# Kernel tuning notes

Measured on AMD Instinct MI355X. Metric: run time of the kernel, lower is better.

Reference implementation:

```python
import jax, jax.numpy as jnp
import numpy as np

# B groups, N packed tokens/group, D model dim, H heads, L layers, FF mlp hidden,
# M samples packed per group, C classes, PD patch_dim, NF/NT freq/time pos tables
B, N, D, H, L, FF, M, C, PD, NF, NT = 4, 1024, 768, 12, 12, 3072, 8, 527, 256, 8, 64


def _ln(x, g, b, eps=1e-6):
    m = jnp.mean(x, -1, keepdims=True)
    v = jnp.mean((x - m) ** 2, -1, keepdims=True)
    return (x - m) * jax.lax.rsqrt(v + eps) * g + b


def _attn(xq, xkv, Wq, bq, Wkv, bkv, Wo, bo, allowed):
    # allowed: [b, i, j] bool; faithful to source: NO 1/sqrt(d_head) scaling.
    b, i, _ = xq.shape
    j = xkv.shape[1]
    q = (xq @ Wq + bq).reshape(b, i, H, -1).transpose(0, 2, 1, 3)
    k, v = jnp.split(xkv @ Wkv + bkv, 2, axis=-1)
    k = k.reshape(b, j, H, -1).transpose(0, 2, 1, 3)
    v = v.reshape(b, j, H, -1).transpose(0, 2, 1, 3)
    dots = jnp.einsum('bhid,bhjd->bhij', q, k)
    neg = -jnp.finfo(dots.dtype).max
    dots = jnp.where(allowed[:, None, :, :], dots, neg)
    a = jax.nn.softmax(dots, axis=-1)
    out = jnp.einsum('bhij,bhjd->bhid', a, v).transpose(0, 2, 1, 3).reshape(b, i, -1)
    return out @ Wo + bo


def setup_inputs() -> dict:
    ks = iter(jax.random.split(jax.random.key(0), 48))
    rn = lambda shape, s=0.02: jax.random.normal(next(ks), shape, jnp.float32) * s
    return {
        'patches': jax.random.normal(next(ks), (B, N, PD), jnp.float32),
        'sample_ids': jnp.sort(jax.random.randint(next(ks), (B, N), 0, M), axis=-1).astype(jnp.int32),
        'key_pad': jnp.ones((B, N), bool),
        'freq_idx': jax.random.randint(next(ks), (B, N), 0, NF).astype(jnp.int32),
        'time_idx': jax.random.randint(next(ks), (B, N), 0, NT).astype(jnp.int32),
        'patch_W': rn((PD, D)), 'patch_b': jnp.zeros((D,)),
        'pos_f': rn((NF, D), 1.0), 'pos_t': rn((NT, D), 1.0),
        'ln1_g': jnp.ones((L, D)), 'ln1_b': jnp.zeros((L, D)),
        'Wq': rn((L, D, D)), 'bq': jnp.zeros((L, D)),
        'Wkv': rn((L, D, 2 * D)), 'bkv': jnp.zeros((L, 2 * D)),
        'Wo': rn((L, D, D)), 'bo': jnp.zeros((L, D)),
        'ln2_g': jnp.ones((L, D)), 'ln2_b': jnp.zeros((L, D)),
        'W1': rn((L, D, FF)), 'b1': jnp.zeros((L, FF)),
        'W2': rn((L, FF, D)), 'b2': jnp.zeros((L, D)),
        'norm_g': jnp.ones((D,)), 'norm_b': jnp.zeros((D,)),
        'pool_q': rn((D,), 1.0),
        'pool_Wq': rn((D, D)), 'pool_bq': jnp.zeros((D,)),
        'pool_Wkv': rn((D, 2 * D)), 'pool_bkv': jnp.zeros((2 * D,)),
        'pool_Wo': rn((D, D)), 'pool_bo': jnp.zeros((D,)),
        'mln_g': jnp.ones((D,)), 'mln_b': jnp.zeros((D,)),
        'head_W': rn((D, C)), 'head_b': jnp.zeros((C,)),
    }


def reference(patches, sample_ids, key_pad, freq_idx, time_idx, patch_W, patch_b, pos_f, pos_t,
              ln1_g, ln1_b, Wq, bq, Wkv, bkv, Wo, bo, ln2_g, ln2_b, W1, b1, W2, b2,
              norm_g, norm_b, pool_q, pool_Wq, pool_bq, pool_Wkv, pool_bkv, pool_Wo, pool_bo,
              mln_g, mln_b, head_W, head_b):
    # patch embed + factorized freq/time positional embedding
    x = patches @ patch_W + patch_b + pos_f[freq_idx] + pos_t[time_idx]  # [B, N, D]
    # block-diagonal attention within each packed sample + key-padding mask
    same = sample_ids[:, :, None] == sample_ids[:, None, :]
    allowed = same & key_pad[:, None, :]
    for l in range(L):
        h = _ln(x, ln1_g[l], ln1_b[l])
        x = x + _attn(h, h, Wq[l], bq[l], Wkv[l], bkv[l], Wo[l], bo[l], allowed)
        h = _ln(x, ln2_g[l], ln2_b[l])
        x = x + (jax.nn.gelu(h @ W1[l] + b1[l], approximate=False) @ W2[l] + b2[l])
    x = _ln(x, norm_g, norm_b)
    # attention pooling: one learned query per packed sample, attends only its own tokens
    queries = jnp.broadcast_to(pool_q, (B, M, D))
    pool_allowed = (sample_ids[:, None, :] == jnp.arange(M)[None, :, None]) & key_pad[:, None, :]
    pooled = _attn(queries, x, pool_Wq, pool_bq, pool_Wkv, pool_bkv, pool_Wo, pool_bo, pool_allowed)
    return _ln(pooled, mln_g, mln_b) @ head_W + head_b  # [B, M, C]
```

## Files before the change

kernel.cpp:

```cpp
#include <hip/hip_runtime.h>
#include <hip/hip_bf16.h>
#include <math.h>

#define BB   4
#define NN   1024
#define DD   768
#define HHH  12
#define LLL  12
#define FFD  3072
#define MMM  8
#define CCC  527
#define PDIM 256

typedef unsigned short u16;
typedef __attribute__((ext_vector_type(8))) short bf16x8;
typedef __attribute__((ext_vector_type(4))) float f32x4;

__device__ inline float b2f(u16 x) {
    union { float f; unsigned u; } c; c.u = ((unsigned)x) << 16; return c.f;
}
__device__ inline u16 f2b(float f) {
    __hip_bfloat16 h = __float2bfloat16(f);
    return *reinterpret_cast<u16*>(&h);
}

__device__ __forceinline__ void gl_lds16(const u16* g, const u16* l) {
    __builtin_amdgcn_global_load_lds(
        (const __attribute__((address_space(1))) unsigned int*)(unsigned long long)g,
        (__attribute__((address_space(3))) unsigned int*)(unsigned)(unsigned long long)l,
        16, 0, 0);
}

__global__ void k_pad_norm(const void* __restrict__ p, unsigned char* __restrict__ out, int n) {
    __shared__ int isInt;
    const int t = threadIdx.x;
    if (t == 0) isInt = 1;
    __syncthreads();
    const unsigned* up = (const unsigned*)p;
    for (int i = t; i < n / 4; i += 1024) {
        unsigned v = up[i];
        if (v > 1u) isInt = 0;
    }
    __syncthreads();
    const int* ip = (const int*)p;
    const unsigned char* cp = (const unsigned char*)p;
    const int mode = isInt;
    for (int i = t; i < n; i += 1024)
        out[i] = mode ? (unsigned char)(ip[i] != 0) : (unsigned char)(cp[i] != 0);
}

__global__ __launch_bounds__(256) void k_transpose_cvt(
    const float* __restrict__ src, u16* __restrict__ dst,
    int K, int N, long srcLS, long dstLS)
{
    __shared__ float t[32][33];
    const float* s = src + (size_t)blockIdx.z * srcLS;
    u16* d = dst + (size_t)blockIdx.z * dstLS;
    int n0 = blockIdx.x * 32, k0 = blockIdx.y * 32;
    int tx = threadIdx.x & 31, ty = threadIdx.x >> 5;
    #pragma unroll
    for (int i = 0; i < 32; i += 8)
        t[ty + i][tx] = s[(size_t)(k0 + ty + i) * N + n0 + tx];
    __syncthreads();
    #pragma unroll
    for (int i = 0; i < 32; i += 8)
        d[(size_t)(n0 + ty + i) * K + k0 + tx] = f2b(t[tx][ty + i]);
}

__global__ __launch_bounds__(256) void k_cvt(const float* __restrict__ s, u16* __restrict__ d, int n4) {
    int i = blockIdx.x * 256 + threadIdx.x;
    if (i >= n4) return;
    float4 v = ((const float4*)s)[i];
    union { u16 h[4]; uint2 u; } o;
    o.h[0] = f2b(v.x); o.h[1] = f2b(v.y); o.h[2] = f2b(v.z); o.h[3] = f2b(v.w);
    ((uint2*)d)[i] = o.u;
}

__global__ __launch_bounds__(256) void k_bias_pack(const float* __restrict__ bq,
                                                   const float* __restrict__ bkv,
                                                   float* __restrict__ bqkv) {
    int i = blockIdx.x * 256 + threadIdx.x;
    if (i >= LLL * 2304) return;
    int l = i / 2304, c = i % 2304;
    bqkv[i] = (c < 768) ? bq[l * 768 + c] : bkv[l * 1536 + (c - 768)];
}

__global__ void k_ranges(const int* __restrict__ sid, int2* __restrict__ qr, int2* __restrict__ pr) {
    int b = blockIdx.x, t = threadIdx.x;
    const int* s = sid + b * NN;
    if (t < 16) {
        int lo_id = s[t * 64], hi_id = s[t * 64 + 63];
        int lo = 0, hi = NN;
        while (lo < hi) { int mid = (lo + hi) >> 1; if (s[mid] < lo_id) lo = mid + 1; else hi = mid; }
        int l2 = 0, h2 = NN;
        while (l2 < h2) { int mid = (l2 + h2) >> 1; if (s[mid] <= hi_id) l2 = mid + 1; else h2 = mid; }
        qr[b * 16 + t] = make_int2(lo, l2);
    }
    if (t < MMM) {
        int l2 = 0, h2 = NN;
        while (l2 < h2) { int mid = (l2 + h2) >> 1; if (s[mid] < t) l2 = mid + 1; else h2 = mid; }
        int l3 = 0, h3 = NN;
        while (l3 < h3) { int mid = (l3 + h3) >> 1; if (s[mid] <= t) l3 = mid + 1; else h3 = mid; }
        pr[b * MMM + t] = make_int2(l2, l3);
    }
}

__device__ inline void stv(u16* p, float v) { *p = f2b(v); }
__device__ inline void stv(float* p, float v) { *p = v; }

template <typename OT>
__global__ __launch_bounds__(256) void k_ln(const float* __restrict__ x,
                                            const float* __restrict__ g,
                                            const float* __restrict__ b,
                                            OT* __restrict__ out) {
    int row = blockIdx.x;
    const float* xr = x + (size_t)row * DD;
    int t = threadIdx.x;
    float v[3], s1 = 0.f, s2 = 0.f;
    #pragma unroll
    for (int i = 0; i < 3; i++) { v[i] = xr[t + i * 256]; s1 += v[i]; s2 += v[i] * v[i]; }
    #pragma unroll
    for (int o = 32; o; o >>= 1) { s1 += __shfl_xor(s1, o); s2 += __shfl_xor(s2, o); }
    __shared__ float a1[4], a2[4];
    int w = t >> 6;
    if ((t & 63) == 0) { a1[w] = s1; a2[w] = s2; }
    __syncthreads();
    s1 = a1[0] + a1[1] + a1[2] + a1[3];
    s2 = a2[0] + a2[1] + a2[2] + a2[3];
    float mean = s1 * (1.f / DD);
    float var = s2 * (1.f / DD) - mean * mean;
    float rstd = rsqrtf(fmaxf(var, 0.f) + 1e-6f);
    #pragma unroll
    for (int i = 0; i < 3; i++) {
        int c = t + i * 256;
        stv(&out[(size_t)row * DD + c], (v[i] - mean) * rstd * g[c] + b[c]);
    }
}

template <int EPI, int BM>
__global__ __launch_bounds__(256) void k_gemm(
    const u16* __restrict__ A, int lda,
    const u16* __restrict__ Bt, int ldb,
    const float* __restrict__ bias,
    float* __restrict__ Cf, u16* __restrict__ Cb,
    const float* __restrict__ resid,
    int ldc, int K)
{
    constexpr int NR = (BM == 128) ? 4 : 2;
    __shared__ __align__(16) u16 As[BM * 32];
    __shared__ __align__(16) u16 Bs[128 * 32];
    const int row0 = blockIdx.y * BM, col0 = blockIdx.x * 128;
    const int t = threadIdx.x;
    const int w = t >> 6, lane = t & 63;
    const int wr = (BM == 128) ? (w >> 1) * 64 : 0;
    const int wc = (BM == 128) ? (w & 1) * 64 : w * 32;
    const int fr = lane & 15, fg = lane >> 4;
    const int srow = t >> 2, sseg = (t & 3) * 8;
    const u16* Ap = A + (size_t)(row0 + srow) * lda + sseg;
    const u16* Bp = Bt + (size_t)(col0 + srow) * ldb + sseg;
    const size_t lstep = (size_t)64 * lda, bstep = (size_t)64 * ldb;

    f32x4 acc[4][NR];
    #pragma unroll
    for (int m = 0; m < 4; m++)
        #pragma unroll
        for (int n = 0; n < NR; n++) acc[m][n] = (f32x4){0.f, 0.f, 0.f, 0.f};

    for (int k0 = 0; k0 < K; k0 += 32) {
        #pragma unroll
        for (int i = 0; i < BM / 64; i++)
            gl_lds16(Ap + i * lstep + k0, As + i * 2048 + t * 8);
        #pragma unroll
        for (int i = 0; i < 2; i++)
            gl_lds16(Bp + i * bstep + k0, Bs + i * 2048 + t * 8);
        __syncthreads();
        bf16x8 af[4], bfr[NR];
        #pragma unroll
        for (int m = 0; m < 4; m++) af[m] = *(const bf16x8*)&As[(wr + m * 16 + fr) * 32 + fg * 8];
        #pragma unroll
        for (int n = 0; n < NR; n++) bfr[n] = *(const bf16x8*)&Bs[(wc + n * 16 + fr) * 32 + fg * 8];
        #pragma unroll
        for (int m = 0; m < 4; m++)
            #pragma unroll
            for (int n = 0; n < NR; n++)
                acc[m][n] = __builtin_amdgcn_mfma_f32_16x16x32_bf16(af[m], bfr[n], acc[m][n], 0, 0, 0);
        __syncthreads();
    }
    #pragma unroll
    for (int m = 0; m < 4; m++) {
        #pragma unroll
        for (int n = 0; n < NR; n++) {
            const int col = col0 + wc + n * 16 + fr;
            const float bb = bias[col];
            #pragma unroll
            for (int r = 0; r < 4; r++) {
                const size_t row = row0 + wr + m * 16 + fg * 4 + r;
                float v = acc[m][n][r] + bb;
                if (EPI == 0) {
                    Cb[row * ldc + col] = f2b(v);
                } else if (EPI == 1) {
                    Cf[row * ldc + col] = v + resid[row * ldc + col];
                } else if (EPI == 2) {
                    float gl = 0.5f * v * (1.f + erff(v * 0.70710678118f));
                    Cb[row * ldc + col] = f2b(gl);
                } else {
                    Cf[row * ldc + col] = v;
                }
            }
        }
    }
}

__global__ __launch_bounds__(256) void k_attn(
    const u16* __restrict__ qkv,
    const int* __restrict__ sid, const unsigned char* __restrict__ pad,
    const int2* __restrict__ qr,
    u16* __restrict__ outb)
{
    __shared__ __align__(16) u16 Qs[64][72];
    __shared__ __align__(16) u16 Ks[64][72];
    __shared__ __align__(16) u16 Vt[64][72];
    __shared__ __align__(16) u16 Ps[4][16][72];
    __shared__ int sidq[64];
    __shared__ int sidj[64];
    __shared__ int padj[64];
    const int b = blockIdx.z, h = blockIdx.y, qt = blockIdx.x;
    const int i0 = qt * 64;
    const int t = threadIdx.x, w = t >> 6, lane = t & 63;
    const int fr = lane & 15, fg = lane >> 4;
    const int srow = t >> 2, sseg = (t & 3) * 16;
    const size_t tokbase = (size_t)b * NN;
    const u16* qbase = qkv + (tokbase + i0) * 2304 + h * 64;
    *(uint4*)&Qs[srow][sseg]     = *(const uint4*)(qbase + (size_t)srow * 2304 + sseg);
    *(uint4*)&Qs[srow][sseg + 8] = *(const uint4*)(qbase + (size_t)srow * 2304 + sseg + 8);
    if (t < 64) sidq[t] = sid[tokbase + i0 + t];
    __syncthreads();
    bf16x8 qf0 = *(const bf16x8*)&Qs[w * 16 + fr][fg * 8];
    bf16x8 qf1 = *(const bf16x8*)&Qs[w * 16 + fr][32 + fg * 8];
    const int myrow = w * 16 + fg * 4;
    float m_run[4], l_run[4];
    f32x4 oacc[4];
    #pragma unroll
    for (int r = 0; r < 4; r++) { m_run[r] = -1e30f; l_run[r] = 0.f; }
    #pragma unroll
    for (int n = 0; n < 4; n++) oacc[n] = (f32x4){0.f, 0.f, 0.f, 0.f};
    const int2 rg = qr[b * 16 + qt];
    const u16* kbase = qkv + tokbase * 2304 + 768 + h * 64;
    const u16* vbase = qkv + tokbase * 2304 + 1536 + h * 64;

    for (int j0 = rg.x & ~63; j0 < rg.y; j0 += 64) {
        __syncthreads();
        *(uint4*)&Ks[srow][sseg]     = *(const uint4*)(kbase + (size_t)(j0 + srow) * 2304 + sseg);
        *(uint4*)&Ks[srow][sseg + 8] = *(const uint4*)(kbase + (size_t)(j0 + srow) * 2304 + sseg + 8);
        {
            uint4 v0 = *(const uint4*)(vbase + (size_t)(j0 + srow) * 2304 + sseg);
            uint4 v1 = *(const uint4*)(vbase + (size_t)(j0 + srow) * 2304 + sseg + 8);
            u16 tmp[16];
            *(uint4*)&tmp[0] = v0;
            *(uint4*)&tmp[8] = v1;
            #pragma unroll
            for (int e = 0; e < 16; e++) Vt[sseg + e][srow] = tmp[e];
        }
        if (t < 64) {
            sidj[t] = sid[tokbase + j0 + t];
            padj[t] = pad[tokbase + j0 + t];
        }
        __syncthreads();
        f32x4 s[4];
        #pragma unroll
        for (int nj = 0; nj < 4; nj++) {
            bf16x8 kf0 = *(const bf16x8*)&Ks[nj * 16 + fr][fg * 8];
            bf16x8 kf1 = *(const bf16x8*)&Ks[nj * 16 + fr][32 + fg * 8];
            f32x4 a = (f32x4){0.f, 0.f, 0.f, 0.f};
            a = __builtin_amdgcn_mfma_f32_16x16x32_bf16(qf0, kf0, a, 0, 0, 0);
            a = __builtin_amdgcn_mfma_f32_16x16x32_bf16(qf1, kf1, a, 0, 0, 0);
            s[nj] = a;
        }
        #pragma unroll
        for (int nj = 0; nj < 4; nj++) {
            const int jj = nj * 16 + fr;
            const int sj = sidj[jj];
            const int pd = padj[jj];
            #pragma unroll
            for (int r = 0; r < 4; r++) {
                const bool ok = pd && (sj == sidq[myrow + r]);
                s[nj][r] = ok ? s[nj][r] : -3e38f;
            }
        }
        float mnew[4], scale[4];
        #pragma unroll
        for (int r = 0; r < 4; r++) {
            float mx = fmaxf(fmaxf(s[0][r], s[1][r]), fmaxf(s[2][r], s[3][r]));
            #pragma unroll
            for (int o = 1; o < 16; o <<= 1) mx = fmaxf(mx, __shfl_xor(mx, o));
            mnew[r] = fmaxf(m_run[r], mx);
            scale[r] = __expf(m_run[r] - mnew[r]);
            m_run[r] = mnew[r];
        }
        #pragma unroll
        for (int r = 0; r < 4; r++) {
            float rs = 0.f;
            #pragma unroll
            for (int nj = 0; nj < 4; nj++) {
                float pv = __expf(s[nj][r] - mnew[r]);
                rs += pv;
                Ps[w][fg * 4 + r][nj * 16 + fr] = f2b(pv);
            }
            #pragma unroll
            for (int o = 1; o < 16; o <<= 1) rs += __shfl_xor(rs, o);
            l_run[r] = l_run[r] * scale[r] + rs;
        }
        #pragma unroll
        for (int n = 0; n < 4; n++)
            #pragma unroll
            for (int r = 0; r < 4; r++) oacc[n][r] *= scale[r];
        bf16x8 pa0 = *(const bf16x8*)&Ps[w][fr][fg * 8];
        bf16x8 pa1 = *(const bf16x8*)&Ps[w][fr][32 + fg * 8];
        #pragma unroll
        for (int nd = 0; nd < 4; nd++) {
            bf16x8 vf0 = *(const bf16x8*)&Vt[nd * 16 + fr][fg * 8];
            bf16x8 vf1 = *(const bf16x8*)&Vt[nd * 16 + fr][32 + fg * 8];
            oacc[nd] = __builtin_amdgcn_mfma_f32_16x16x32_bf16(pa0, vf0, oacc[nd], 0, 0, 0);
            oacc[nd] = __builtin_amdgcn_mfma_f32_16x16x32_bf16(pa1, vf1, oacc[nd], 0, 0, 0);
        }
    }
    float inv[4];
    #pragma unroll
    for (int r = 0; r < 4; r++) inv[r] = 1.f / l_run[r];
    #pragma unroll
    for (int nd = 0; nd < 4; nd++)
        #pragma unroll
        for (int r = 0; r < 4; r++)
            outb[(tokbase + i0 + myrow + r) * DD + h * 64 + nd * 16 + fr] = f2b(oacc[nd][r] * inv[r]);
}

__global__ __launch_bounds__(256) void k_posadd(float* __restrict__ x,
                                                const int* __restrict__ fidx, const int* __restrict__ tidx,
                                                const float* __restrict__ pf, const float* __restrict__ pt) {
    int row = blockIdx.x;
    int fi = fidx[row], ti = tidx[row];
    for (int c = threadIdx.x; c < DD; c += 256)
        x[(size_t)row * DD + c] += pf[(size_t)fi * DD + c] + pt[(size_t)ti * DD + c];
}

__global__ __launch_bounds__(64) void k_qvec(const float* __restrict__ pq, const float* __restrict__ Wq,
                                             const float* __restrict__ bq, float* __restrict__ qv) {
    int c = blockIdx.x;
    int l = threadIdx.x;
    float s = 0.f;
    #pragma unroll
    for (int d = l; d < DD; d += 64) s += pq[d] * Wq[(size_t)d * DD + c];
    #pragma unroll
    for (int o = 32; o; o >>= 1) s += __shfl_xor(s, o);
    if (l == 0) qv[c] = s + bq[c];
}

__global__ __launch_bounds__(256) void k_pool_attn(
    const float* __restrict__ qv, const u16* __restrict__ kv,
    const unsigned char* __restrict__ pad, const int2* __restrict__ pr,
    float* __restrict__ outp)
{
    const int idx = blockIdx.x;
    const int h = idx % HHH, bm = idx / HHH;
    const int b = bm >> 3, m = bm & 7;
    const int2 rg = pr[b * MMM + m];
    const int lo = rg.x, cnt = rg.y - rg.x;
    __shared__ float sc[NN];
    __shared__ float qsh[64];
    __shared__ float rbuf[4];
    __shared__ float vacc[4][64];
    if (threadIdx.x < 64) qsh[threadIdx.x] = qv[h * 64 + threadIdx.x];
    __syncthreads();
    for (int j = threadIdx.x; j < cnt; j += 256) {
        const u16* krow = kv + (size_t)(b * NN + lo + j) * 1536 + h * 64;
        float s = 0.f;
        #pragma unroll
        for (int dv = 0; dv < 8; dv++) {
            bf16x8 k8 = *(const bf16x8*)(krow + dv * 8);
            #pragma unroll
            for (int e = 0; e < 8; e++) s += qsh[dv * 8 + e] * b2f((u16)k8[e]);
        }
        sc[j] = pad[b * NN + lo + j] ? s : -3e38f;
    }
    __syncthreads();
    float mx = -3e38f;
    for (int j = threadIdx.x; j < cnt; j += 256) mx = fmaxf(mx, sc[j]);
    #pragma unroll
    for (int o = 32; o; o >>= 1) mx = fmaxf(mx, __shfl_xor(mx, o));
    if ((threadIdx.x & 63) == 0) rbuf[threadIdx.x >> 6] = mx;
    __syncthreads();
    mx = fmaxf(fmaxf(rbuf[0], rbuf[1]), fmaxf(rbuf[2], rbuf[3]));
    __syncthreads();
    float sm = 0.f;
    for (int j = threadIdx.x; j < cnt; j += 256) { float p = __expf(sc[j] - mx); sc[j] = p; sm += p; }
    #pragma unroll
    for (int o = 32; o; o >>= 1) sm += __shfl_xor(sm, o);
    if ((threadIdx.x & 63) == 0) rbuf[threadIdx.x >> 6] = sm;
    __syncthreads();
    sm = rbuf[0] + rbuf[1] + rbuf[2] + rbuf[3];
    const float inv = 1.f / sm;
    {
        const int d = threadIdx.x & 63, g = threadIdx.x >> 6;
        float acc = 0.f;
        for (int j = g; j < cnt; j += 4)
            acc += sc[j] * b2f(kv[(size_t)(b * NN + lo + j) * 1536 + 768 + h * 64 + d]);
        vacc[g][d] = acc;
        __syncthreads();
        if (g == 0)
            outp[(size_t)(b * MMM + m) * DD + h * 64 + d] =
                (vacc[0][d] + vacc[1][d] + vacc[2][d] + vacc[3][d]) * inv;
    }
}

__global__ __launch_bounds__(256) void k_small_mm(const float* __restrict__ A, const float* __restrict__ W,
                                                  const float* __restrict__ bias, float* __restrict__ out,
                                                  int N, int Kd) {
    const int row = blockIdx.y;
    const int cl = threadIdx.x & 63, kg = threadIdx.x >> 6;
    const int c = blockIdx.x * 64 + cl;
    const int cload = (c < N) ? c : (N - 1);
    __shared__ float As[DD];
    __shared__ float red[4][64];
    for (int d = threadIdx.x; d < Kd; d += 256) As[d] = A[(size_t)row * Kd + d];
    __syncthreads();
    const int kper = Kd >> 2;
    const int kbase = kg * kper;
    float s = 0.f;
    const float* w = W + (size_t)kbase * N + cload;
    #pragma unroll 4
    for (int i = 0; i < kper; i++) s += As[kbase + i] * w[(size_t)i * N];
    red[kg][cl] = s;
    __syncthreads();
    if (kg == 0 && c < N)
        out[(size_t)row * N + c] = red[0][cl] + red[1][cl] + red[2][cl] + red[3][cl] + bias[c];
}

extern "C" void kernel_launch(void* const* d_in, const int* in_sizes, int n_in,
                              void* d_out, int out_size, void* d_ws, size_t ws_size,
                              hipStream_t stream) {
    const float* patches   = (const float*)d_in[0];
    const int*   sample_ids= (const int*)d_in[1];
    const void*  key_pad_raw = (const void*)d_in[2];
    const int*   freq_idx  = (const int*)d_in[3];
    const int*   time_idx  = (const int*)d_in[4];
    const float* patch_W   = (const float*)d_in[5];
    const float* patch_b   = (const float*)d_in[6];
    const float* pos_f     = (const float*)d_in[7];
    const float* pos_t     = (const float*)d_in[8];
    const float* ln1_g     = (const float*)d_in[9];
    const float* ln1_b     = (const float*)d_in[10];
    const float* Wq        = (const float*)d_in[11];
    const float* bq        = (const float*)d_in[12];
    const float* Wkv       = (const float*)d_in[13];
    const float* bkv       = (const float*)d_in[14];
    const float* Wo        = (const float*)d_in[15];
    const float* bo        = (const float*)d_in[16];
    const float* ln2_g     = (const float*)d_in[17];
    const float* ln2_b     = (const float*)d_in[18];
    const float* W1        = (const float*)d_in[19];
    const float* b1        = (const float*)d_in[20];
    const float* W2        = (const float*)d_in[21];
    const float* b2        = (const float*)d_in[22];
    const float* norm_g    = (const float*)d_in[23];
    const float* norm_b    = (const float*)d_in[24];
    const float* pool_q    = (const float*)d_in[25];
    const float* pool_Wq   = (const float*)d_in[26];
    const float* pool_bq   = (const float*)d_in[27];
    const float* pool_Wkv  = (const float*)d_in[28];
    const float* pool_bkv  = (const float*)d_in[29];
    const float* pool_Wo   = (const float*)d_in[30];
    const float* pool_bo   = (const float*)d_in[31];
    const float* mln_g     = (const float*)d_in[32];
    const float* mln_b     = (const float*)d_in[33];
    const float* head_W    = (const float*)d_in[34];
    const float* head_b    = (const float*)d_in[35];
    float* outp = (float*)d_out;
    (void)in_sizes; (void)n_in; (void)out_size; (void)ws_size;

    char* ws = (char*)d_ws;
    size_t off = 0;
    auto alloc = [&](size_t bytes) -> void* {
        void* p = (void*)(ws + off);
        off += (bytes + 255) & ~(size_t)255;
        return p;
    };
    u16* WqkvT    = (u16*)alloc((size_t)LLL * 2304 * 768 * 2);
    u16* WoT      = (u16*)alloc((size_t)LLL * 768 * 768 * 2);
    u16* W1T      = (u16*)alloc((size_t)LLL * 3072 * 768 * 2);
    u16* W2T      = (u16*)alloc((size_t)LLL * 768 * 3072 * 2);
    u16* patchWT  = (u16*)alloc((size_t)768 * 256 * 2);
    u16* poolWkvT = (u16*)alloc((size_t)1536 * 768 * 2);
    float* bqkv   = (float*)alloc((size_t)LLL * 2304 * 4);
    unsigned char* pad_u8 = (unsigned char*)alloc(BB * NN);
    float* x      = (float*)alloc((size_t)4096 * 768 * 4);
    u16* hbuf     = (u16*)alloc((size_t)4096 * 768 * 2);
    u16* qkvb     = (u16*)alloc((size_t)4096 * 2304 * 2);
    u16* attno    = (u16*)alloc((size_t)4096 * 768 * 2);
    u16* mid      = (u16*)alloc((size_t)4096 * 3072 * 2);
    u16* patch_bf = mid;
    u16* xn       = attno;
    u16* poolkv   = qkvb;
    float* qvec   = (float*)alloc(768 * 4);
    float* pooled_pre = (float*)alloc(32 * 768 * 4);
    float* pooled2    = (float*)alloc(32 * 768 * 4);
    float* mlnout     = (float*)alloc(32 * 768 * 4);
    int2* qr = (int2*)alloc(4 * 16 * sizeof(int2));
    int2* pr = (int2*)alloc(4 * 8 * sizeof(int2));

    k_pad_norm<<<1, 1024, 0, stream>>>(key_pad_raw, pad_u8, BB * NN);
    k_transpose_cvt<<<dim3(24, 24, LLL), 256, 0, stream>>>(Wq, WqkvT, 768, 768, (long)768 * 768, (long)2304 * 768);
    k_transpose_cvt<<<dim3(48, 24, LLL), 256, 0, stream>>>(Wkv, WqkvT + (size_t)768 * 768, 768, 1536, (long)768 * 1536, (long)2304 * 768);
    k_transpose_cvt<<<dim3(24, 24, LLL), 256, 0, stream>>>(Wo, WoT, 768, 768, (long)768 * 768, (long)768 * 768);
    k_transpose_cvt<<<dim3(96, 24, LLL), 256, 0, stream>>>(W1, W1T, 768, 3072, (long)768 * 3072, (long)3072 * 768);
    k_transpose_cvt<<<dim3(24, 96, LLL), 256, 0, stream>>>(W2, W2T, 3072, 768, (long)3072 * 768, (long)768 * 3072);
    k_transpose_cvt<<<dim3(24, 8, 1), 256, 0, stream>>>(patch_W, patchWT, 256, 768, 0, 0);
    k_transpose_cvt<<<dim3(48, 24, 1), 256, 0, stream>>>(pool_Wkv, poolWkvT, 768, 1536, 0, 0);
    k_cvt<<<1024, 256, 0, stream>>>(patches, patch_bf, 4096 * 256 / 4);
    k_bias_pack<<<(LLL * 2304 + 255) / 256, 256, 0, stream>>>(bq, bkv, bqkv);
    k_ranges<<<4, 64, 0, stream>>>(sample_ids, qr, pr);

    k_gemm<3, 64><<<dim3(6, 64), 256, 0, stream>>>(patch_bf, 256, patchWT, 256, patch_b, x, nullptr, nullptr, 768, 256);
    k_posadd<<<4096, 256, 0, stream>>>(x, freq_idx, time_idx, pos_f, pos_t);

    for (int l = 0; l < LLL; l++) {
        k_ln<u16><<<4096, 256, 0, stream>>>(x, ln1_g + l * 768, ln1_b + l * 768, hbuf);
        k_gemm<0, 128><<<dim3(18, 32), 256, 0, stream>>>(hbuf, 768, WqkvT + (size_t)l * 2304 * 768, 768,
                                                         bqkv + l * 2304, nullptr, qkvb, nullptr, 2304, 768);
        k_attn<<<dim3(16, 12, 4), 256, 0, stream>>>(qkvb, sample_ids, pad_u8, qr, attno);
        k_gemm<1, 64><<<dim3(6, 64), 256, 0, stream>>>(attno, 768, WoT + (size_t)l * 768 * 768, 768,
                                                       bo + l * 768, x, nullptr, x, 768, 768);
        k_ln<u16><<<4096, 256, 0, stream>>>(x, ln2_g + l * 768, ln2_b + l * 768, hbuf);
        k_gemm<2, 128><<<dim3(24, 32), 256, 0, stream>>>(hbuf, 768, W1T + (size_t)l * 3072 * 768, 768,
                                                         b1 + l * 3072, nullptr, mid, nullptr, 3072, 768);
        k_gemm<1, 64><<<dim3(6, 64), 256, 0, stream>>>(mid, 3072, W2T + (size_t)l * 768 * 3072, 3072,
                                                       b2 + l * 768, x, nullptr, x, 768, 3072);
    }

    k_ln<u16><<<4096, 256, 0, stream>>>(x, norm_g, norm_b, xn);
    k_gemm<0, 128><<<dim3(12, 32), 256, 0, stream>>>(xn, 768, poolWkvT, 768, pool_bkv, nullptr, poolkv, nullptr, 1536, 768);
    k_qvec<<<768, 64, 0, stream>>>(pool_q, pool_Wq, pool_bq, qvec);
    k_pool_attn<<<BB * MMM * HHH, 256, 0, stream>>>(qvec, poolkv, pad_u8, pr, pooled_pre);
    k_small_mm<<<dim3(12, 32), 256, 0, stream>>>(pooled_pre, pool_Wo, pool_bo, pooled2, 768, 768);
    k_ln<float><<<32, 256, 0, stream>>>(pooled2, mln_g, mln_b, mlnout);
    k_small_mm<<<dim3(9, 32), 256, 0, stream>>>(mlnout, head_W, head_b, outp, 527, 768);
}
```

Baseline: 2.491 ms.

## Triple-buffer GEMM LDS tiles with async prefetch two k-steps ahead

Replaces the single-buffered load-sync-compute-sync loop in the bf16 MFMA GEMM with a three-stage LDS ring. Tiles are prefetched two k-iterations ahead, and an explicit vmcnt wait plus one barrier per iteration replaces the two __syncthreads. The aim is to overlap global-to-LDS traffic with MFMA work and remove one barrier per step. It triples LDS use, which may cut occupancy, and it depends on hand-counted vmcnt values matching the number of outstanding loads.

```diff
diff --git a/kernel.cpp b/kernel.cpp
--- a/kernel.cpp
+++ b/kernel.cpp
@@ -146,9 +146,11 @@
     const float* __restrict__ resid,
     int ldc, int K)
 {
-    constexpr int NR = (BM == 128) ? 4 : 2;
-    __shared__ __align__(16) u16 As[BM * 32];
-    __shared__ __align__(16) u16 Bs[128 * 32];
+    constexpr int NR  = (BM == 128) ? 4 : 2;
+    constexpr int ASZ = BM * 32;
+    constexpr int BSZ = 128 * 32;
+    __shared__ __align__(16) u16 As[3][ASZ];
+    __shared__ __align__(16) u16 Bs[3][BSZ];
     const int row0 = blockIdx.y * BM, col0 = blockIdx.x * 128;
     const int t = threadIdx.x;
     const int w = t >> 6, lane = t & 63;
@@ -160,31 +162,46 @@
     const u16* Bp = Bt + (size_t)(col0 + srow) * ldb + sseg;
     const size_t lstep = (size_t)64 * lda, bstep = (size_t)64 * ldb;
 
+    auto stage = [&](int buf, int k0) {
+        #pragma unroll
+        for (int i = 0; i < BM / 64; i++)
+            gl_lds16(Ap + i * lstep + k0, &As[buf][i * 2048 + t * 8]);
+        #pragma unroll
+        for (int i = 0; i < 2; i++)
+            gl_lds16(Bp + i * bstep + k0, &Bs[buf][i * 2048 + t * 8]);
+    };
+
     f32x4 acc[4][NR];
     #pragma unroll
     for (int m = 0; m < 4; m++)
         #pragma unroll
         for (int n = 0; n < NR; n++) acc[m][n] = (f32x4){0.f, 0.f, 0.f, 0.f};
 
-    for (int k0 = 0; k0 < K; k0 += 32) {
-        #pragma unroll
-        for (int i = 0; i < BM / 64; i++)
-            gl_lds16(Ap + i * lstep + k0, As + i * 2048 + t * 8);
-        #pragma unroll
-        for (int i = 0; i < 2; i++)
-            gl_lds16(Bp + i * bstep + k0, Bs + i * 2048 + t * 8);
-        __syncthreads();
+    const int nt = K >> 5;
+    stage(0, 0);
+    stage(1, 32);
+
+    for (int kt = 0; kt < nt; ++kt) {
+        if (kt + 1 < nt) {
+            if constexpr (BM == 128) asm volatile("s_waitcnt vmcnt(4)" ::: "memory");
+            else                     asm volatile("s_waitcnt vmcnt(3)" ::: "memory");
+        } else {
+            asm volatile("s_waitcnt vmcnt(0)" ::: "memory");
+        }
+        __builtin_amdgcn_s_barrier();
+        __builtin_amdgcn_sched_barrier(0);
+        if (kt + 2 < nt) stage((kt + 2) % 3, (kt + 2) * 32);
+        const int cur = kt % 3;
         bf16x8 af[4], bfr[NR];
         #pragma unroll
-        for (int m = 0; m < 4; m++) af[m] = *(const bf16x8*)&As[(wr + m * 16 + fr) * 32 + fg * 8];
-        #pragma unroll
-        for (int n = 0; n < NR; n++) bfr[n] = *(const bf16x8*)&Bs[(wc + n * 16 + fr) * 32 + fg * 8];
+        for (int m = 0; m < 4; m++) af[m] = *(const bf16x8*)&As[cur][(wr + m * 16 + fr) * 32 + fg * 8];
+        #pragma unroll
+        for (int n = 0; n < NR; n++) bfr[n] = *(const bf16x8*)&Bs[cur][(wc + n * 16 + fr) * 32 + fg * 8];
         #pragma unroll
         for (int m = 0; m < 4; m++)
             #pragma unroll
             for (int n = 0; n < NR; n++)
                 acc[m][n] = __builtin_amdgcn_mfma_f32_16x16x32_bf16(af[m], bfr[n], acc[m][n], 0, 0, 0);
-        __syncthreads();
     }
     #pragma unroll
     for (int m = 0; m < 4; m++) {
```

New measurement: 2.178 ms. 1.14x faster.
